# Performance work log

Hardware: AMD Instinct MI355X
Metric: run time of the kernel (lower is better)

Reference implementation:

```python
import jax, jax.numpy as jnp
import numpy as np

B, SQ, SK, D, DV = 16, 2048, 2048, 128, 128
NUM_HEADS = 2
DROPOUT_P = 0.1
SCALE_FACTOR = 1.0 / (DROPOUT_P * NUM_HEADS)  # = 5.0; scores are divided by this


def setup_inputs() -> dict:
    key = jax.random.key(0)
    k1, k2, k3, k4 = jax.random.split(key, 4)
    x1 = jax.random.normal(k1, (B, SQ, D), dtype=jnp.float32)
    x2 = jax.random.normal(k2, (B, SK, D), dtype=jnp.float32)
    x3 = jax.random.normal(k3, (B, SK, DV), dtype=jnp.float32)
    # deterministic dropout keep-mask (True -> keep), keep prob = 1 - p
    drop_mask = jax.random.bernoulli(k4, 1.0 - DROPOUT_P, (B, SQ, SK))
    return {"x1": x1, "x2": x2, "x3": x3, "drop_mask": drop_mask}


def reference(x1, x2, x3, drop_mask):
    # v1 = x1 @ x2^T : [B, Sq, Sk]
    scores = jnp.einsum("bqd,bkd->bqk", x1, x2)
    # v2 = v1 / scale_factor (scale_factor = 1/(p*heads) = 5 -> multiply by 0.2)
    scores = scores * (1.0 / SCALE_FACTOR)
    probs = jax.nn.softmax(scores, axis=-1)
    # dropout with inverted scaling 1/(1-p)
    keep_scale = 1.0 / (1.0 - DROPOUT_P)
    probs = jnp.where(drop_mask, probs * keep_scale, 0.0)
    # output = probs @ x3 : [B, Sq, Dv]
    return jnp.einsum("bqk,bkv->bqv", probs, x3)
```

## Files before the change

### kernel.cpp

```cpp
#include <hip/hip_runtime.h>
#include <stdint.h>


#define B_   16
#define SQ_  2048
#define SK_  2048
#define D_   128
#define DV_  128

#define BQ   64
#define BK   64
#define NTILE 32
#define LDQ  136
#define LDK  136
#define LDP  72
#define LDV2 36

typedef short  s16x8 __attribute__((ext_vector_type(8)));
typedef float  f32x4 __attribute__((ext_vector_type(4)));
typedef unsigned short u16;
typedef unsigned int   u32;
typedef u32 u32x4 __attribute__((ext_vector_type(4)));

__device__ __forceinline__ u16 f2bf(float f) {
    u32 u = __builtin_bit_cast(u32, f);
    u = (u + 0x7FFFu + ((u >> 16) & 1u)) >> 16;
    return (u16)u;
}
__device__ __forceinline__ u32 pk2(float a, float b) {
    return (u32)f2bf(a) | ((u32)f2bf(b) << 16);
}
__device__ __forceinline__ u32x4 ntld(const int* p) {
#if __has_builtin(__builtin_nontemporal_load)
    return __builtin_nontemporal_load((const u32x4*)p);
#else
    return *(const u32x4*)p;
#endif
}
__device__ __forceinline__ u32 mpack(u32 m0, u32 m1) {
    return ((0u - m0) & 0xFFFFu) | ((0u - m1) << 16);
}

#define MFMA(a, b, c) __builtin_amdgcn_mfma_f32_16x16x32_bf16((a), (b), (c), 0, 0, 0)

__global__ __launch_bounds__(256, 2)
void fattn_kernel(const float* __restrict__ Qg, const float* __restrict__ Kg,
                  const float* __restrict__ Vg, const int* __restrict__ Mg,
                  float* __restrict__ Og)
{
    __shared__ unsigned char smem[53248];
    u16* Qs  = (u16*)smem;
    u16* Ps  = (u16*)smem;
    u16* Ks  = (u16*)(smem + 17408);
    u32* Vt  = (u32*)(smem + 34816);

    const int tid  = threadIdx.x;
    const int wave = tid >> 6;
    const int lane = tid & 63;
    const int n16  = lane & 15;
    const int quad = lane >> 4;

    const int b  = blockIdx.x >> 5;
    const int q0 = (blockIdx.x & 31) << 6;

    const int srow = tid >> 4;
    const int scol = (tid & 15) * 8;
    const int vl   = tid & 31;
    const int vdv0 = vl * 4;
    const int vko  = tid >> 5;
    const int vrot = 4 * (vl & 7) + 16 * ((vl >> 3) & 1);

    {
        const float* src = Qg + ((size_t)b * SQ_ + q0) * D_;
        #pragma unroll
        for (int c = 0; c < 4; ++c) {
            int row = c * 16 + srow;
            float4 v0 = *(const float4*)(&src[row * D_ + scol]);
            float4 v1 = *(const float4*)(&src[row * D_ + scol + 4]);
            uint4 pk = { pk2(v0.x, v0.y), pk2(v0.z, v0.w),
                         pk2(v1.x, v1.y), pk2(v1.z, v1.w) };
            *(uint4*)(&Qs[row * LDQ + scol]) = pk;
        }
    }
    __syncthreads();

    s16x8 aQ[4];
    #pragma unroll
    for (int kb = 0; kb < 4; ++kb)
        aQ[kb] = *(const s16x8*)(&Qs[(wave * 16 + n16) * LDQ + kb * 32 + quad * 8]);

    int vt0[8], vt1[8];
    #pragma unroll
    for (int nt = 0; nt < 8; ++nt) {
        int dv  = nt * 16 + n16;
        int rot = 4 * ((dv >> 2) & 7) + 16 * ((dv >> 5) & 1);
        int col = (quad * 4 + rot) & 31;
        vt0[nt] = dv * LDV2 + col;
        vt1[nt] = dv * LDV2 + (col ^ 16);
    }

    f32x4 o[8];
    #pragma unroll
    for (int i = 0; i < 8; ++i) o[i] = (f32x4){0.f, 0.f, 0.f, 0.f};
    float l_part[4] = {0.f, 0.f, 0.f, 0.f};

    const int* mrowp = Mg + (size_t)(b * SQ_ + q0 + wave * 16 + n16) * SK_
                          + quad * 8;

    const float* pK = Kg + (size_t)b * SK_ * D_;
    const float* pV = Vg + (size_t)b * SK_ * DV_;

    float4 ka[4], kb4[4], va4[4], vb4[4];
    #pragma unroll
    for (int c = 0; c < 4; ++c) {
        int row = c * 16 + srow;
        ka[c]  = *(const float4*)(&pK[row * D_ + scol]);
        kb4[c] = *(const float4*)(&pK[row * D_ + scol + 4]);
    }
    #pragma unroll
    for (int g = 0; g < 4; ++g) {
        int row = g * 16 + vko * 2;
        va4[g] = *(const float4*)(&pV[row * DV_ + vdv0]);
        vb4[g] = *(const float4*)(&pV[(row + 1) * DV_ + vdv0]);
    }

    for (int it = 0; it < NTILE; ++it) {
        __syncthreads();

        const int* mp = mrowp + it * BK;
        u32x4 am0 = ntld(mp);
        u32x4 am1 = ntld(mp + 4);
        u32x4 am2 = ntld(mp + 32);
        u32x4 am3 = ntld(mp + 36);

        #pragma unroll
        for (int c = 0; c < 4; ++c) {
            int row = c * 16 + srow;
            uint4 pk = { pk2(ka[c].x, ka[c].y),     pk2(ka[c].z, ka[c].w),
                         pk2(kb4[c].x, kb4[c].y),   pk2(kb4[c].z, kb4[c].w) };
            *(uint4*)(&Ks[row * LDK + scol]) = pk;
        }
        #pragma unroll
        for (int g = 0; g < 4; ++g) {
            int w = (g * 8 + vko + vrot) & 31;
            u32* vp = &Vt[vdv0 * LDV2 + w];
            vp[0]      = pk2(va4[g].x, vb4[g].x);
            vp[LDV2]   = pk2(va4[g].y, vb4[g].y);
            vp[2*LDV2] = pk2(va4[g].z, vb4[g].z);
            vp[3*LDV2] = pk2(va4[g].w, vb4[g].w);
        }

        if (it + 1 < NTILE) {
            const float* nK = pK + (size_t)(it + 1) * BK * D_;
            const float* nV = pV + (size_t)(it + 1) * BK * DV_;
            #pragma unroll
            for (int c = 0; c < 4; ++c) {
                int row = c * 16 + srow;
                ka[c]  = *(const float4*)(&nK[row * D_ + scol]);
                kb4[c] = *(const float4*)(&nK[row * D_ + scol + 4]);
            }
            #pragma unroll
            for (int g = 0; g < 4; ++g) {
                int row = g * 16 + vko * 2;
                va4[g] = *(const float4*)(&nV[row * DV_ + vdv0]);
                vb4[g] = *(const float4*)(&nV[(row + 1) * DV_ + vdv0]);
            }
        }

        __syncthreads();

        f32x4 s[4];
        #pragma unroll
        for (int t = 0; t < 4; ++t) s[t] = (f32x4){0.f, 0.f, 0.f, 0.f};
        #pragma unroll
        for (int kb = 0; kb < 4; ++kb) {
            #pragma unroll
            for (int t = 0; t < 4; ++t) {
                s16x8 bK = *(const s16x8*)(&Ks[(t * 16 + n16) * LDK + kb * 32 + quad * 8]);
                s[t] = MFMA(aQ[kb], bK, s[t]);
            }
        }

        #pragma unroll
        for (int t = 0; t < 4; ++t)
            #pragma unroll
            for (int r = 0; r < 4; ++r) {
                float p = __expf(fmaf(s[t][r], 0.2f, -12.0f));
                l_part[r] += p;
                Ps[(wave * 16 + quad * 4 + r) * LDP
                   + ((t * 16 + n16 + 16 * quad) & 63)] = f2bf(p);
            }

        #pragma unroll
        for (int kk = 0; kk < 2; ++kk) {
            s16x8 aP = *(const s16x8*)(&Ps[(wave * 16 + n16) * LDP
                        + ((kk * 32 + quad * 8 + 16 * (n16 >> 2)) & 63)]);
            u32x4 f = __builtin_bit_cast(u32x4, aP);
            if (kk == 0) {
                f.x &= mpack(am0.x, am0.y);  f.y &= mpack(am0.z, am0.w);
                f.z &= mpack(am1.x, am1.y);  f.w &= mpack(am1.z, am1.w);
            } else {
                f.x &= mpack(am2.x, am2.y);  f.y &= mpack(am2.z, am2.w);
                f.z &= mpack(am3.x, am3.y);  f.w &= mpack(am3.z, am3.w);
            }
            s16x8 aPm = __builtin_bit_cast(s16x8, f);
            #pragma unroll
            for (int nt = 0; nt < 8; ++nt) {
                s16x8 bV = *(const s16x8*)(&Vt[kk ? vt1[nt] : vt0[nt]]);
                o[nt] = MFMA(aPm, bV, o[nt]);
            }
        }
    }

    const float keep_scale = 1.0f / 0.9f;
    #pragma unroll
    for (int r = 0; r < 4; ++r) {
        float l = l_part[r];
        l += __shfl_xor(l, 1); l += __shfl_xor(l, 2);
        l += __shfl_xor(l, 4); l += __shfl_xor(l, 8);
        float inv_l = keep_scale / l;
        size_t obase = ((size_t)b * SQ_ + q0 + wave * 16 + quad * 4 + r) * DV_;
        #pragma unroll
        for (int nt = 0; nt < 8; ++nt)
            Og[obase + nt * 16 + n16] = o[nt][r] * inv_l;
    }
}

extern "C" void kernel_launch(void* const* d_in, const int* in_sizes, int n_in,
                              void* d_out, int out_size, void* d_ws, size_t ws_size,
                              hipStream_t stream) {
    const float* Qg = (const float*)d_in[0];
    const float* Kg = (const float*)d_in[1];
    const float* Vg = (const float*)d_in[2];
    const int*   Mg = (const int*)d_in[3];
    float* Og = (float*)d_out;
    dim3 grid(B_ * (SQ_ / BQ));
    fattn_kernel<<<grid, 256, 0, stream>>>(Qg, Kg, Vg, Mg, Og);
}
```

Measured before the change: 450.5 us.

## Pre-convert K and transposed V to bf16 in workspace before attention

Adds two prepass kernels that convert K to bf16 and V to a transposed bf16 layout in the workspace. The attention kernel then streams half the bytes per K/V tile and copies them straight into shared memory, with no per-tile fp32-to-bf16 packing or scattered transpose stores. In exchange there are two extra launches and extra global traffic, since each K/V element is written once and read back. The original fp32 path is kept as a fallback when the workspace is too small.

```diff
diff --git a/kernel.cpp b/kernel.cpp
--- a/kernel.cpp
+++ b/kernel.cpp
@@ -43,10 +43,57 @@
 
 #define MFMA(a, b, c) __builtin_amdgcn_mfma_f32_16x16x32_bf16((a), (b), (c), 0, 0, 0)
 
+__global__ __launch_bounds__(256, 4)
+void convK_kernel(const float* __restrict__ Kg, u16* __restrict__ Kb)
+{
+    size_t i = ((size_t)blockIdx.x * 256 + threadIdx.x) * 8;
+    float4 a = *(const float4*)(Kg + i);
+    float4 c = *(const float4*)(Kg + i + 4);
+    uint4 o = { pk2(a.x, a.y), pk2(a.z, a.w), pk2(c.x, c.y), pk2(c.z, c.w) };
+    *(uint4*)(Kb + i) = o;
+}
+
 __global__ __launch_bounds__(256, 2)
-void fattn_kernel(const float* __restrict__ Qg, const float* __restrict__ Kg,
-                  const float* __restrict__ Vg, const int* __restrict__ Mg,
-                  float* __restrict__ Og)
+void convV_kernel(const float* __restrict__ Vg, u16* __restrict__ Vtg)
+{
+    __shared__ u16 Vs[64 * 136];
+    const int tid  = threadIdx.x;
+    const int b    = blockIdx.x >> 5;
+    const int k0   = (blockIdx.x & 31) << 6;
+    const int srow = tid >> 4;
+    const int scol = (tid & 15) * 8;
+
+    const float* src = Vg + ((size_t)b * SK_ + k0) * DV_;
+    #pragma unroll
+    for (int c = 0; c < 4; ++c) {
+        int row = c * 16 + srow;
+        float4 v0 = *(const float4*)(&src[row * DV_ + scol]);
+        float4 v1 = *(const float4*)(&src[row * DV_ + scol + 4]);
+        uint4 pk = { pk2(v0.x, v0.y), pk2(v0.z, v0.w),
+                     pk2(v1.x, v1.y), pk2(v1.z, v1.w) };
+        *(uint4*)(&Vs[row * 136 + scol]) = pk;
+    }
+    __syncthreads();
+
+    u16* dst = Vtg + (size_t)b * DV_ * SK_;
+    #pragma unroll
+    for (int u = 0; u < 4; ++u) {
+        int dv = 32 * u + (tid >> 3);
+        int kg = tid & 7;
+        u16 v[8];
+        #pragma unroll
+        for (int j = 0; j < 8; ++j)
+            v[j] = Vs[(kg * 8 + j) * 136 + dv];
+        uint4 o = { (u32)v[0] | ((u32)v[1] << 16), (u32)v[2] | ((u32)v[3] << 16),
+                    (u32)v[4] | ((u32)v[5] << 16), (u32)v[6] | ((u32)v[7] << 16) };
+        *(uint4*)(dst + (size_t)dv * SK_ + k0 + kg * 8) = o;
+    }
+}
+
+__global__ __launch_bounds__(256, 2)
+void fattn_bf16(const float* __restrict__ Qg, const u16* __restrict__ Kb,
+                const u16* __restrict__ Vtg, const int* __restrict__ Mg,
+                float* __restrict__ Og)
 {
     __shared__ unsigned char smem[53248];
     u16* Qs  = (u16*)smem;
@@ -56,19 +103,17 @@
 
     const int tid  = threadIdx.x;
     const int wave = tid >> 6;
-    const int lane = tid & 63;
-    const int n16  = lane & 15;
-    const int quad = lane >> 4;
+    const int n16  = tid & 15;
+    const int quad = (tid & 63) >> 4;
 
     const int b  = blockIdx.x >> 5;
     const int q0 = (blockIdx.x & 31) << 6;
 
     const int srow = tid >> 4;
     const int scol = (tid & 15) * 8;
-    const int vl   = tid & 31;
-    const int vdv0 = vl * 4;
-    const int vko  = tid >> 5;
-    const int vrot = 4 * (vl & 7) + 16 * ((vl >> 3) & 1);
+    const int vdvs = tid >> 3;
+    const int vkg  = tid & 7;
+    const int wbase = (4 * vkg + 4 * ((tid >> 5) & 7)) & 31;
 
     {
         const float* src = Qg + ((size_t)b * SQ_ + q0) * D_;
@@ -107,22 +152,16 @@
     const int* mrowp = Mg + (size_t)(b * SQ_ + q0 + wave * 16 + n16) * SK_
                           + quad * 8;
 
-    const float* pK = Kg + (size_t)b * SK_ * D_;
-    const float* pV = Vg + (size_t)b * SK_ * DV_;
-
-    float4 ka[4], kb4[4], va4[4], vb4[4];
-    #pragma unroll
-    for (int c = 0; c < 4; ++c) {
-        int row = c * 16 + srow;
-        ka[c]  = *(const float4*)(&pK[row * D_ + scol]);
-        kb4[c] = *(const float4*)(&pK[row * D_ + scol + 4]);
-    }
-    #pragma unroll
-    for (int g = 0; g < 4; ++g) {
-        int row = g * 16 + vko * 2;
-        va4[g] = *(const float4*)(&pV[row * DV_ + vdv0]);
-        vb4[g] = *(const float4*)(&pV[(row + 1) * DV_ + vdv0]);
-    }
+    const u16* pK = Kb  + (size_t)b * SK_ * D_;
+    const u16* pV = Vtg + (size_t)b * DV_ * SK_;
+
+    uint4 kun[4], vun[4];
+    #pragma unroll
+    for (int c = 0; c < 4; ++c)
+        kun[c] = *(const uint4*)(&pK[(c * 16 + srow) * D_ + scol]);
+    #pragma unroll
+    for (int u = 0; u < 4; ++u)
+        vun[u] = *(const uint4*)(&pV[(size_t)(32 * u + vdvs) * SK_ + vkg * 8]);
 
     for (int it = 0; it < NTILE; ++it) {
         __syncthreads();
@@ -134,37 +173,24 @@
         u32x4 am3 = ntld(mp + 36);
 
         #pragma unroll
-        for (int c = 0; c < 4; ++c) {
-            int row = c * 16 + srow;
-            uint4 pk = { pk2(ka[c].x, ka[c].y),     pk2(ka[c].z, ka[c].w),
-                         pk2(kb4[c].x, kb4[c].y),   pk2(kb4[c].z, kb4[c].w) };
-            *(uint4*)(&Ks[row * LDK + scol]) = pk;
-        }
-        #pragma unroll
-        for (int g = 0; g < 4; ++g) {
-            int w = (g * 8 + vko + vrot) & 31;
-            u32* vp = &Vt[vdv0 * LDV2 + w];
-            vp[0]      = pk2(va4[g].x, vb4[g].x);
-            vp[LDV2]   = pk2(va4[g].y, vb4[g].y);
-            vp[2*LDV2] = pk2(va4[g].z, vb4[g].z);
-            vp[3*LDV2] = pk2(va4[g].w, vb4[g].w);
+        for (int c = 0; c < 4; ++c)
+            *(uint4*)(&Ks[(c * 16 + srow) * LDK + scol]) = kun[c];
+        #pragma unroll
+        for (int u = 0; u < 4; ++u) {
+            int dv = 32 * u + vdvs;
+            int w  = (wbase + 16 * (u & 1)) & 31;
+            *(uint4*)(&Vt[dv * LDV2 + w]) = vun[u];
         }
 
         if (it + 1 < NTILE) {
-            const float* nK = pK + (size_t)(it + 1) * BK * D_;
-            const float* nV = pV + (size_t)(it + 1) * BK * DV_;
-            #pragma unroll
-            for (int c = 0; c < 4; ++c) {
-                int row = c * 16 + srow;
-                ka[c]  = *(const float4*)(&nK[row * D_ + scol]);
-                kb4[c] = *(const float4*)(&nK[row * D_ + scol + 4]);
-            }
-            #pragma unroll
-            for (int g = 0; g < 4; ++g) {
-                int row = g * 16 + vko * 2;
-                va4[g] = *(const float4*)(&nV[row * DV_ + vdv0]);
-                vb4[g] = *(const float4*)(&nV[(row + 1) * DV_ + vdv0]);
-            }
+            const u16* nK = pK + (size_t)(it + 1) * BK * D_;
+            const u16* nV = pV + (size_t)(it + 1) * BK;
+            #pragma unroll
+            for (int c = 0; c < 4; ++c)
+                kun[c] = *(const uint4*)(&nK[(c * 16 + srow) * D_ + scol]);
+            #pragma unroll
+            for (int u = 0; u < 4; ++u)
+                vun[u] = *(const uint4*)(&nV[(size_t)(32 * u + vdvs) * SK_ + vkg * 8]);
         }
 
         __syncthreads();
@@ -226,6 +252,178 @@
     }
 }
 
+__global__ __launch_bounds__(256, 2)
+void fattn_f32(const float* __restrict__ Qg, const float* __restrict__ Kg,
+               const float* __restrict__ Vg, const int* __restrict__ Mg,
+               float* __restrict__ Og)
+{
+    __shared__ unsigned char smem[53248];
+    u16* Qs  = (u16*)smem;
+    u16* Ps  = (u16*)smem;
+    u16* Ks  = (u16*)(smem + 17408);
+    u32* Vt  = (u32*)(smem + 34816);
+
+    const int tid  = threadIdx.x;
+    const int wave = tid >> 6;
+    const int n16  = tid & 15;
+    const int quad = (tid & 63) >> 4;
+    const int b  = blockIdx.x >> 5;
+    const int q0 = (blockIdx.x & 31) << 6;
+    const int srow = tid >> 4;
+    const int scol = (tid & 15) * 8;
+    const int vl   = tid & 31;
+    const int vdv0 = vl * 4;
+    const int vko  = tid >> 5;
+    const int vrot = 4 * (vl & 7) + 16 * ((vl >> 3) & 1);
+
+    {
+        const float* src = Qg + ((size_t)b * SQ_ + q0) * D_;
+        #pragma unroll
+        for (int c = 0; c < 4; ++c) {
+            int row = c * 16 + srow;
+            float4 v0 = *(const float4*)(&src[row * D_ + scol]);
+            float4 v1 = *(const float4*)(&src[row * D_ + scol + 4]);
+            uint4 pk = { pk2(v0.x, v0.y), pk2(v0.z, v0.w),
+                         pk2(v1.x, v1.y), pk2(v1.z, v1.w) };
+            *(uint4*)(&Qs[row * LDQ + scol]) = pk;
+        }
+    }
+    __syncthreads();
+
+    s16x8 aQ[4];
+    #pragma unroll
+    for (int kb = 0; kb < 4; ++kb)
+        aQ[kb] = *(const s16x8*)(&Qs[(wave * 16 + n16) * LDQ + kb * 32 + quad * 8]);
+
+    int vt0[8], vt1[8];
+    #pragma unroll
+    for (int nt = 0; nt < 8; ++nt) {
+        int dv  = nt * 16 + n16;
+        int rot = 4 * ((dv >> 2) & 7) + 16 * ((dv >> 5) & 1);
+        int col = (quad * 4 + rot) & 31;
+        vt0[nt] = dv * LDV2 + col;
+        vt1[nt] = dv * LDV2 + (col ^ 16);
+    }
+
+    f32x4 o[8];
+    #pragma unroll
+    for (int i = 0; i < 8; ++i) o[i] = (f32x4){0.f, 0.f, 0.f, 0.f};
+    float l_part[4] = {0.f, 0.f, 0.f, 0.f};
+    const int* mrowp = Mg + (size_t)(b * SQ_ + q0 + wave * 16 + n16) * SK_ + quad * 8;
+    const float* pK = Kg + (size_t)b * SK_ * D_;
+    const float* pV = Vg + (size_t)b * SK_ * DV_;
+
+    float4 ka[4], kb4[4], va4[4], vb4[4];
+    #pragma unroll
+    for (int c = 0; c < 4; ++c) {
+        int row = c * 16 + srow;
+        ka[c]  = *(const float4*)(&pK[row * D_ + scol]);
+        kb4[c] = *(const float4*)(&pK[row * D_ + scol + 4]);
+    }
+    #pragma unroll
+    for (int g = 0; g < 4; ++g) {
+        int row = g * 16 + vko * 2;
+        va4[g] = *(const float4*)(&pV[row * DV_ + vdv0]);
+        vb4[g] = *(const float4*)(&pV[(row + 1) * DV_ + vdv0]);
+    }
+
+    for (int it = 0; it < NTILE; ++it) {
+        __syncthreads();
+        const int* mp = mrowp + it * BK;
+        u32x4 am0 = ntld(mp);
+        u32x4 am1 = ntld(mp + 4);
+        u32x4 am2 = ntld(mp + 32);
+        u32x4 am3 = ntld(mp + 36);
+
+        #pragma unroll
+        for (int c = 0; c < 4; ++c) {
+            int row = c * 16 + srow;
+            uint4 pk = { pk2(ka[c].x, ka[c].y),     pk2(ka[c].z, ka[c].w),
+                         pk2(kb4[c].x, kb4[c].y),   pk2(kb4[c].z, kb4[c].w) };
+            *(uint4*)(&Ks[row * LDK + scol]) = pk;
+        }
+        #pragma unroll
+        for (int g = 0; g < 4; ++g) {
+            int w = (g * 8 + vko + vrot) & 31;
+            u32* vp = &Vt[vdv0 * LDV2 + w];
+            vp[0]      = pk2(va4[g].x, vb4[g].x);
+            vp[LDV2]   = pk2(va4[g].y, vb4[g].y);
+            vp[2*LDV2] = pk2(va4[g].z, vb4[g].z);
+            vp[3*LDV2] = pk2(va4[g].w, vb4[g].w);
+        }
+        if (it + 1 < NTILE) {
+            const float* nK = pK + (size_t)(it + 1) * BK * D_;
+            const float* nV = pV + (size_t)(it + 1) * BK * DV_;
+            #pragma unroll
+            for (int c = 0; c < 4; ++c) {
+                int row = c * 16 + srow;
+                ka[c]  = *(const float4*)(&nK[row * D_ + scol]);
+                kb4[c] = *(const float4*)(&nK[row * D_ + scol + 4]);
+            }
+            #pragma unroll
+            for (int g = 0; g < 4; ++g) {
+                int row = g * 16 + vko * 2;
+                va4[g] = *(const float4*)(&nV[row * DV_ + vdv0]);
+                vb4[g] = *(const float4*)(&nV[(row + 1) * DV_ + vdv0]);
+            }
+        }
+        __syncthreads();
+
+        f32x4 s[4];
+        #pragma unroll
+        for (int t = 0; t < 4; ++t) s[t] = (f32x4){0.f, 0.f, 0.f, 0.f};
+        #pragma unroll
+        for (int kb = 0; kb < 4; ++kb) {
+            #pragma unroll
+            for (int t = 0; t < 4; ++t) {
+                s16x8 bK = *(const s16x8*)(&Ks[(t * 16 + n16) * LDK + kb * 32 + quad * 8]);
+                s[t] = MFMA(aQ[kb], bK, s[t]);
+            }
+        }
+        #pragma unroll
+        for (int t = 0; t < 4; ++t)
+            #pragma unroll
+            for (int r = 0; r < 4; ++r) {
+                float p = __expf(fmaf(s[t][r], 0.2f, -12.0f));
+                l_part[r] += p;
+                Ps[(wave * 16 + quad * 4 + r) * LDP
+                   + ((t * 16 + n16 + 16 * quad) & 63)] = f2bf(p);
+            }
+        #pragma unroll
+        for (int kk = 0; kk < 2; ++kk) {
+            s16x8 aP = *(const s16x8*)(&Ps[(wave * 16 + n16) * LDP
+                        + ((kk * 32 + quad * 8 + 16 * (n16 >> 2)) & 63)]);
+            u32x4 f = __builtin_bit_cast(u32x4, aP);
+            if (kk == 0) {
+                f.x &= mpack(am0.x, am0.y);  f.y &= mpack(am0.z, am0.w);
+                f.z &= mpack(am1.x, am1.y);  f.w &= mpack(am1.z, am1.w);
+            } else {
+                f.x &= mpack(am2.x, am2.y);  f.y &= mpack(am2.z, am2.w);
+                f.z &= mpack(am3.x, am3.y);  f.w &= mpack(am3.z, am3.w);
+            }
+            s16x8 aPm = __builtin_bit_cast(s16x8, f);
+            #pragma unroll
+            for (int nt = 0; nt < 8; ++nt) {
+                s16x8 bV = *(const s16x8*)(&Vt[kk ? vt1[nt] : vt0[nt]]);
+                o[nt] = MFMA(aPm, bV, o[nt]);
+            }
+        }
+    }
+
+    const float keep_scale = 1.0f / 0.9f;
+    #pragma unroll
+    for (int r = 0; r < 4; ++r) {
+        float l = l_part[r];
+        l += __shfl_xor(l, 1); l += __shfl_xor(l, 2);
+        l += __shfl_xor(l, 4); l += __shfl_xor(l, 8);
+        float inv_l = keep_scale / l;
+        size_t obase = ((size_t)b * SQ_ + q0 + wave * 16 + quad * 4 + r) * DV_;
+        #pragma unroll
+        for (int nt = 0; nt < 8; ++nt)
+            Og[obase + nt * 16 + n16] = o[nt][r] * inv_l;
+    }
+}
+
 extern "C" void kernel_launch(void* const* d_in, const int* in_sizes, int n_in,
                               void* d_out, int out_size, void* d_ws, size_t ws_size,
                               hipStream_t stream) {
@@ -234,6 +432,15 @@
     const float* Vg = (const float*)d_in[2];
     const int*   Mg = (const int*)d_in[3];
     float* Og = (float*)d_out;
-    dim3 grid(B_ * (SQ_ / BQ));
-    fattn_kernel<<<grid, 256, 0, stream>>>(Qg, Kg, Vg, Mg, Og);
-}
+
+    const size_t kv_elems = (size_t)B_ * SK_ * D_;
+    if (ws_size >= 2 * kv_elems * sizeof(u16)) {
+        u16* Kb  = (u16*)d_ws;
+        u16* Vtg = Kb + kv_elems;
+        convK_kernel<<<dim3(kv_elems / (256 * 8)), 256, 0, stream>>>(Kg, Kb);
+        convV_kernel<<<dim3(B_ * (SK_ / 64)), 256, 0, stream>>>(Vg, Vtg);
+        fattn_bf16<<<dim3(B_ * (SQ_ / BQ)), 256, 0, stream>>>(Qg, Kb, Vtg, Mg, Og);
+    } else {
+        fattn_f32<<<dim3(B_ * (SQ_ / BQ)), 256, 0, stream>>>(Qg, Kg, Vg, Mg, Og);
+    }
+}
```

Result: slower. 602.7 us (+33.8%).
